# Performance work log

Measured on AMD Instinct MI355X. Metric: run time of the kernel, lower is better.

## Reference

```python
import jax, jax.numpy as jnp
import numpy as np

# ---- HashGridPlanesEncoder config (hybrid-k-planes) ----
NUM_LEVELS = 16
LEVEL_DIM = 2
BASE_RES = 16
DESIRED_RES = 2048
LOG2_HASHMAP = 19
D = 2  # grid_nd: each plane encoder is a 2D hash grid
N_PTS = 1048576
COO_COMBS = [(0, 1), (0, 2), (1, 2)]
HASH_PRIME_1 = 2654435761  # torch-ngp fast_hash prime for dim 1 (dim 0 prime is 1)


def _level_constants():
    # Mirrors torch-ngp GridEncoder offset/resolution computation.
    pls = 2.0 ** (np.log2(DESIRED_RES / BASE_RES) / (NUM_LEVELS - 1))
    max_params = 2 ** LOG2_HASHMAP
    scales, res, sizes, offs = [], [], [], [0]
    for l in range(NUM_LEVELS):
        s = BASE_RES * pls ** l - 1.0          # kernel: scale = exp2(l*S + H) - 1
        r = int(np.ceil(s)) + 1                # kernel: resolution = ceil(scale) + 1
        p = min(max_params, (r + 1) ** D)      # align_corners=False -> (res+1)^D
        p = int(np.ceil(p / 8) * 8)            # round up to multiple of 8
        scales.append(s); res.append(r); sizes.append(p); offs.append(offs[-1] + p)
    return (np.array(scales, np.float32), np.array(res, np.int64),
            np.array(sizes, np.int64), np.array(offs[:-1], np.int64), offs[-1])


SCALES, RES, SIZES, OFFSETS, TOTAL_PARAMS = _level_constants()
USE_HASH = ((RES + 1) ** D) > SIZES  # static per-level: dense linear index vs spatial hash


def _encode_plane(x2, table):
    """x2: [N,2] coords in [0,1]; table: [TOTAL_PARAMS, LEVEL_DIM]. Returns [N, L*C]."""
    n = x2.shape[0]
    scales = jnp.asarray(SCALES)
    pos = x2[:, None, :] * scales[None, :, None] + 0.5           # [N,L,2] (align_corners=False)
    pg_f = jnp.floor(pos)
    frac = pos - pg_f                                            # [N,L,2]
    pg = pg_f.astype(jnp.uint32)
    corners = jnp.array([[0, 0], [1, 0], [0, 1], [1, 1]], jnp.uint32)  # [4,2]
    cpos = pg[:, :, None, :] + corners[None, None]               # [N,L,4,2]
    cmask = corners.astype(bool)[None, None]                     # [1,1,4,2]
    w = jnp.where(cmask, frac[:, :, None, :], 1.0 - frac[:, :, None, :]).prod(-1)  # [N,L,4]
    stride1 = jnp.asarray((RES + 1).astype(np.uint32))           # [L]
    linear = cpos[..., 0] + cpos[..., 1] * stride1[None, :, None]
    hashed = cpos[..., 0] ^ (cpos[..., 1] * jnp.uint32(HASH_PRIME_1))  # uint32 wrap-around
    idx = jnp.where(jnp.asarray(USE_HASH)[None, :, None], hashed, linear)
    idx = idx % jnp.asarray(SIZES.astype(np.uint32))[None, :, None]
    idx = (idx + jnp.asarray(OFFSETS.astype(np.uint32))[None, :, None]).astype(jnp.int32)
    feats = table[idx]                                           # [N,L,4,C] gather
    out = (w[..., None] * feats).sum(axis=2)                     # [N,L,C] bilinear interp
    return out.reshape(n, NUM_LEVELS * LEVEL_DIM)


def setup_inputs() -> dict:
    key = jax.random.key(0)
    kp, k0, k1, k2 = jax.random.split(key, 4)
    pts = jax.random.uniform(kp, (N_PTS, 3), dtype=jnp.float32)  # coords (treated as in [-1,1] domain)
    std = 1e-4  # GridEncoder init: embeddings.uniform_(-1e-4, 1e-4)
    mk = lambda k: jax.random.uniform(k, (TOTAL_PARAMS, LEVEL_DIM), jnp.float32, -std, std)
    return {"pts": pts, "table_xy": mk(k0), "table_xz": mk(k1), "table_yz": mk(k2)}


def reference(pts, table_xy, table_xz, table_yz):
    # GridEncoder.forward normalizes inputs: (x + bound) / (2*bound), bound=1
    u = (pts + 1.0) * 0.5
    tables = (table_xy, table_xz, table_yz)
    out = _encode_plane(u[:, list(COO_COMBS[0])], tables[0])
    for comb, tab in zip(COO_COMBS[1:], tables[1:]):
        out = out + _encode_plane(u[:, list(comb)], tab)
    return out
```

## Files before the change

### kernel.cpp

```cpp
#include <hip/hip_runtime.h>
#include <hip/hip_fp16.h>
#include <cmath>

#define NLEV 16
#define HASH_START 12
#define HMASK ((1u << 19) - 1u)
#define HASH_PRIME 2654435761u
#define LDS_WORDS 14160

typedef float    f4 __attribute__((ext_vector_type(4)));
typedef unsigned u4 __attribute__((ext_vector_type(4)));

struct LvlC {
  float scale[NLEV];
  unsigned stride[NLEV];
  unsigned offset[NLEV];
};

__device__ __forceinline__ float2 h2f(unsigned u) {
  return __half22float2(__builtin_bit_cast(__half2, u));
}
__device__ __forceinline__ void nt_store4(float* p, float a, float b, float c, float d) {
  f4 v = {a, b, c, d};
  __builtin_nontemporal_store(v, reinterpret_cast<f4*>(p));
}

__global__ __launch_bounds__(256) void k_convert(
    const float2* __restrict__ t0, const float2* __restrict__ t1,
    const float2* __restrict__ t2, unsigned* __restrict__ dst, unsigned total)
{
  unsigned g = blockIdx.x * 256 + threadIdx.x;
  unsigned stp = gridDim.x * 256;
  unsigned tot3 = 3u * total;
  for (unsigned e = g; e < tot3; e += stp) {
    const float2* src; unsigned i = e;
    if (i < total)            { src = t0; }
    else if (i < 2u * total)  { src = t1; i -= total; }
    else                      { src = t2; i -= 2u * total; }
    float2 v = src[i];
    __half2 h = __floats2half2_rn(v.x, v.y);
    __builtin_nontemporal_store(__builtin_bit_cast(unsigned, h), dst + e);
  }
}

__global__ __launch_bounds__(256) void k_dense1011(
    const float* __restrict__ pts, const unsigned* __restrict__ tab,
    unsigned* __restrict__ s10, unsigned* __restrict__ s11,
    LvlC lc, unsigned total, int half)
{
  int t = blockIdx.x * 256 + threadIdx.x;
  if (t >= half) return;
  const int idx[2] = {t, t + half};

  float ua[2][3], ub[2][3];
#pragma unroll
  for (int k = 0; k < 2; ++k) {
    float u0 = (pts[3 * idx[k] + 0] + 1.f) * .5f;
    float u1 = (pts[3 * idx[k] + 1] + 1.f) * .5f;
    float u2 = (pts[3 * idx[k] + 2] + 1.f) * .5f;
    ua[k][0] = u0; ub[k][0] = u1;
    ua[k][1] = u0; ub[k][1] = u2;
    ua[k][2] = u1; ub[k][2] = u2;
  }

  uint2 g[2][2][3][2];
  float rx[2][2][3], ry[2][2][3];
#pragma unroll
  for (int k = 0; k < 2; ++k)
#pragma unroll
    for (int l = 0; l < 2; ++l) {
      const float sc = lc.scale[10 + l];
      const unsigned st = lc.stride[10 + l], o = lc.offset[10 + l];
#pragma unroll
      for (int p = 0; p < 3; ++p) {
        float px = ua[k][p] * sc + .5f, py = ub[k][p] * sc + .5f;
        float fx = floorf(px), fy = floorf(py);
        rx[k][l][p] = px - fx; ry[k][l][p] = py - fy;
        unsigned i00 = (unsigned)fx + (unsigned)fy * st + o;
        const unsigned* tp = tab + (size_t)p * total;
        g[k][l][p][0] = *reinterpret_cast<const uint2*>(tp + i00);
        g[k][l][p][1] = *reinterpret_cast<const uint2*>(tp + i00 + st);
      }
    }

#pragma unroll
  for (int k = 0; k < 2; ++k)
#pragma unroll
    for (int l = 0; l < 2; ++l) {
      float s0 = 0.f, s1 = 0.f;
#pragma unroll
      for (int p = 0; p < 3; ++p) {
        float x = rx[k][l][p], y = ry[k][l][p];
        float w00 = (1.f - x) * (1.f - y), w10 = x * (1.f - y);
        float w01 = (1.f - x) * y,          w11 = x * y;
        float2 f00 = h2f(g[k][l][p][0].x), f10 = h2f(g[k][l][p][0].y);
        float2 f01 = h2f(g[k][l][p][1].x), f11 = h2f(g[k][l][p][1].y);
        s0 += w00 * f00.x + w10 * f10.x + w01 * f01.x + w11 * f11.x;
        s1 += w00 * f00.y + w10 * f10.y + w01 * f01.y + w11 * f11.y;
      }
      unsigned hv = __builtin_bit_cast(unsigned, __floats2half2_rn(s0, s1));
      unsigned* sl = l ? s11 : s10;
      __builtin_nontemporal_store(hv, sl + idx[k]);
    }
}

__global__ __launch_bounds__(256) void k_hash_lvl(
    const float* __restrict__ pts, const unsigned* __restrict__ tab,
    unsigned* __restrict__ slice, float sc, unsigned o, unsigned total, int half)
{
  int t = blockIdx.x * 256 + threadIdx.x;
  if (t >= half) return;
  const int idx[2] = {t, t + half};

  float ua[2][3], ub[2][3];
#pragma unroll
  for (int k = 0; k < 2; ++k) {
    float u0 = (pts[3 * idx[k] + 0] + 1.f) * .5f;
    float u1 = (pts[3 * idx[k] + 1] + 1.f) * .5f;
    float u2 = (pts[3 * idx[k] + 2] + 1.f) * .5f;
    ua[k][0] = u0; ub[k][0] = u1;
    ua[k][1] = u0; ub[k][1] = u2;
    ua[k][2] = u1; ub[k][2] = u2;
  }

  unsigned g[2][3][4];
  float rx[2][3], ry[2][3];
#pragma unroll
  for (int k = 0; k < 2; ++k)
#pragma unroll
    for (int p = 0; p < 3; ++p) {
      float px = ua[k][p] * sc + .5f, py = ub[k][p] * sc + .5f;
      float fx = floorf(px), fy = floorf(py);
      rx[k][p] = px - fx; ry[k][p] = py - fy;
      unsigned x0 = (unsigned)fx, y0 = (unsigned)fy;
      unsigned hy0 = y0 * HASH_PRIME, hy1 = hy0 + HASH_PRIME;
      const unsigned* tp = tab + (size_t)p * total + o;
      g[k][p][0] = tp[(x0 ^ hy0) & HMASK];
      g[k][p][1] = tp[((x0 + 1u) ^ hy0) & HMASK];
      g[k][p][2] = tp[(x0 ^ hy1) & HMASK];
      g[k][p][3] = tp[((x0 + 1u) ^ hy1) & HMASK];
    }

#pragma unroll
  for (int k = 0; k < 2; ++k) {
    float s0 = 0.f, s1 = 0.f;
#pragma unroll
    for (int p = 0; p < 3; ++p) {
      float x = rx[k][p], y = ry[k][p];
      float w00 = (1.f - x) * (1.f - y), w10 = x * (1.f - y);
      float w01 = (1.f - x) * y,          w11 = x * y;
      float2 f00 = h2f(g[k][p][0]), f10 = h2f(g[k][p][1]);
      float2 f01 = h2f(g[k][p][2]), f11 = h2f(g[k][p][3]);
      s0 += w00 * f00.x + w10 * f10.x + w01 * f01.x + w11 * f11.x;
      s1 += w00 * f00.y + w10 * f10.y + w01 * f01.y + w11 * f11.y;
    }
    __builtin_nontemporal_store(
        __builtin_bit_cast(unsigned, __floats2half2_rn(s0, s1)), slice + idx[k]);
  }
}

__global__ __launch_bounds__(256) void k_final(
    const float* __restrict__ pts, const unsigned* __restrict__ tab,
    const unsigned* __restrict__ slices,
    float* __restrict__ out, LvlC lc, unsigned total, int n)
{
  __shared__ unsigned lds[LDS_WORDS];
  int i = blockIdx.x * 256 + threadIdx.x;

  float u0 = (pts[3 * i + 0] + 1.f) * .5f;
  float u1 = (pts[3 * i + 1] + 1.f) * .5f;
  float u2 = (pts[3 * i + 2] + 1.f) * .5f;
  const float ua[3] = {u0, u0, u1}, ub[3] = {u1, u2, u2};

  float res[12];
#pragma unroll
  for (int j = 0; j < 12; ++j) res[j] = 0.f;

  for (int p = 0; p < 3; ++p) {
    if (p) __syncthreads();
    const u4* src = reinterpret_cast<const u4*>(tab + (size_t)p * total);
    for (unsigned e = threadIdx.x; e < LDS_WORDS / 4; e += 256)
      reinterpret_cast<u4*>(lds)[e] = src[e];
    __syncthreads();
#pragma unroll
    for (int l = 0; l < 6; ++l) {
      float px = ua[p] * lc.scale[l] + .5f, py = ub[p] * lc.scale[l] + .5f;
      float fx = floorf(px), fy = floorf(py);
      float x = px - fx, y = py - fy;
      unsigned st = lc.stride[l];
      unsigned i00 = (unsigned)fx + (unsigned)fy * st + lc.offset[l];
      float2 f00 = h2f(lds[i00]),      f10 = h2f(lds[i00 + 1]);
      float2 f01 = h2f(lds[i00 + st]), f11 = h2f(lds[i00 + st + 1]);
      float w00 = (1.f - x) * (1.f - y), w10 = x * (1.f - y);
      float w01 = (1.f - x) * y,          w11 = x * y;
      res[2 * l + 0] += w00 * f00.x + w10 * f10.x + w01 * f01.x + w11 * f11.x;
      res[2 * l + 1] += w00 * f00.y + w10 * f10.y + w01 * f01.y + w11 * f11.y;
    }
  }

  uint2 g[4][3][2];
  float gx[4][3], gy[4][3];
#pragma unroll
  for (int l = 0; l < 4; ++l) {
    const float sc = lc.scale[6 + l];
    const unsigned st = lc.stride[6 + l], o = lc.offset[6 + l];
#pragma unroll
    for (int p = 0; p < 3; ++p) {
      float px = ua[p] * sc + .5f, py = ub[p] * sc + .5f;
      float fx = floorf(px), fy = floorf(py);
      gx[l][p] = px - fx; gy[l][p] = py - fy;
      unsigned i00 = (unsigned)fx + (unsigned)fy * st + o;
      const unsigned* tp = tab + (size_t)p * total;
      g[l][p][0] = *reinterpret_cast<const uint2*>(tp + i00);
      g[l][p][1] = *reinterpret_cast<const uint2*>(tp + i00 + st);
    }
  }
  unsigned sl[6];
#pragma unroll
  for (int j = 0; j < 6; ++j) sl[j] = slices[(size_t)j * n + i];

  float res69[8];
#pragma unroll
  for (int l = 0; l < 4; ++l) {
    float s0 = 0.f, s1 = 0.f;
#pragma unroll
    for (int p = 0; p < 3; ++p) {
      float x = gx[l][p], y = gy[l][p];
      float w00 = (1.f - x) * (1.f - y), w10 = x * (1.f - y);
      float w01 = (1.f - x) * y,          w11 = x * y;
      float2 f00 = h2f(g[l][p][0].x), f10 = h2f(g[l][p][0].y);
      float2 f01 = h2f(g[l][p][1].x), f11 = h2f(g[l][p][1].y);
      s0 += w00 * f00.x + w10 * f10.x + w01 * f01.x + w11 * f11.x;
      s1 += w00 * f00.y + w10 * f10.y + w01 * f01.y + w11 * f11.y;
    }
    res69[2 * l] = s0; res69[2 * l + 1] = s1;
  }

  float v[32];
#pragma unroll
  for (int j = 0; j < 12; ++j) v[j] = res[j];
#pragma unroll
  for (int j = 0; j < 8; ++j) v[12 + j] = res69[j];
#pragma unroll
  for (int j = 0; j < 6; ++j) {
    float2 f = h2f(sl[j]);
    v[20 + 2 * j] = f.x; v[20 + 2 * j + 1] = f.y;
  }
  float* orow = out + (size_t)i * 32;
#pragma unroll
  for (int j = 0; j < 8; ++j)
    nt_store4(orow + 4 * j, v[4 * j], v[4 * j + 1], v[4 * j + 2], v[4 * j + 3]);
}

__global__ __launch_bounds__(256) void k_fallback(
    const float* __restrict__ pts, const float2* __restrict__ txy,
    const float2* __restrict__ txz, const float2* __restrict__ tyz,
    float* __restrict__ out, LvlC lc, int n)
{
  int i = blockIdx.x * 256 + threadIdx.x;
  if (i >= n) return;
  float u0 = (pts[3 * i + 0] + 1.f) * .5f;
  float u1 = (pts[3 * i + 1] + 1.f) * .5f;
  float u2 = (pts[3 * i + 2] + 1.f) * .5f;
  const float ua[3] = {u0, u0, u1}, ub[3] = {u1, u2, u2};
  const float2* tabs[3] = {txy, txz, tyz};
  float acc[32];
#pragma unroll
  for (int j = 0; j < 32; ++j) acc[j] = 0.f;
#pragma unroll
  for (int l = 0; l < NLEV; ++l) {
    const float sc = lc.scale[l];
    const unsigned o = lc.offset[l], s = lc.stride[l];
#pragma unroll
    for (int p = 0; p < 3; ++p) {
      const float2* t = tabs[p];
      float px = ua[p] * sc + .5f, py = ub[p] * sc + .5f;
      float fx = floorf(px), fy = floorf(py);
      float rx = px - fx, ry = py - fy;
      unsigned x0 = (unsigned)fx, y0 = (unsigned)fy;
      float w00 = (1.f - rx) * (1.f - ry), w10 = rx * (1.f - ry);
      float w01 = (1.f - rx) * ry,          w11 = rx * ry;
      float2 f00, f10, f01, f11;
      if (l >= HASH_START) {
        unsigned hy0 = y0 * HASH_PRIME, hy1 = hy0 + HASH_PRIME;
        f00 = t[o + ((x0 ^ hy0) & HMASK)];
        f10 = t[o + (((x0 + 1u) ^ hy0) & HMASK)];
        f01 = t[o + ((x0 ^ hy1) & HMASK)];
        f11 = t[o + (((x0 + 1u) ^ hy1) & HMASK)];
      } else {
        unsigned i00 = x0 + y0 * s;
        float4 r0 = *reinterpret_cast<const float4*>(t + o + i00);
        float4 r1 = *reinterpret_cast<const float4*>(t + o + i00 + s);
        f00 = make_float2(r0.x, r0.y); f10 = make_float2(r0.z, r0.w);
        f01 = make_float2(r1.x, r1.y); f11 = make_float2(r1.z, r1.w);
      }
      acc[2 * l + 0] += w00 * f00.x + w10 * f10.x + w01 * f01.x + w11 * f11.x;
      acc[2 * l + 1] += w00 * f00.y + w10 * f10.y + w01 * f01.y + w11 * f11.y;
    }
  }
  float* orow = out + (size_t)i * 32;
#pragma unroll
  for (int j = 0; j < 8; ++j)
    nt_store4(orow + 4 * j, acc[4 * j], acc[4 * j + 1], acc[4 * j + 2], acc[4 * j + 3]);
}

static unsigned compute_levels(LvlC* lc)
{
  const double pls = std::pow(2.0, std::log2(2048.0 / 16.0) / 15.0);
  unsigned long long off = 0;
  for (int l = 0; l < NLEV; ++l) {
    double s = 16.0 * std::pow(pls, (double)l) - 1.0;
    lc->scale[l] = (float)s;
    long long r = (long long)std::ceil(s) + 1;
    long long dense = (r + 1) * (r + 1);
    long long sz = dense < (1LL << 19) ? dense : (1LL << 19);
    sz = ((sz + 7) / 8) * 8;
    lc->stride[l] = (unsigned)(r + 1);
    lc->offset[l] = (unsigned)off;
    off += (unsigned long long)sz;
  }
  return (unsigned)off;
}

extern "C" void kernel_launch(void* const* d_in, const int* in_sizes, int n_in,
                              void* d_out, int out_size, void* d_ws, size_t ws_size,
                              hipStream_t stream) {
  const float*  pts = (const float*)d_in[0];
  const float2* txy = (const float2*)d_in[1];
  const float2* txz = (const float2*)d_in[2];
  const float2* tyz = (const float2*)d_in[3];
  float* out = (float*)d_out;
  int n = in_sizes[0] / 3;

  LvlC lc;
  unsigned total = compute_levels(&lc);

  size_t tab_bytes = (size_t)3 * total * 4;
  size_t tab_al = (tab_bytes + 255) & ~(size_t)255;
  size_t need = tab_al + (size_t)6 * n * 4;

  bool ok = (n % 512 == 0) && (lc.offset[6] == LDS_WORDS) && (ws_size >= need);
  for (int l = HASH_START; l < NLEV; ++l) {
    unsigned sz = ((l + 1 < NLEV) ? lc.offset[l + 1] : total) - lc.offset[l];
    ok = ok && (sz == (1u << 19));
  }

  int block = 256;
  int grid = (n + block - 1) / block;
  if (!ok) {
    k_fallback<<<grid, block, 0, stream>>>(pts, txy, txz, tyz, out, lc, n);
    return;
  }

  unsigned* tab16 = (unsigned*)d_ws;
  unsigned* slices = (unsigned*)((char*)d_ws + tab_al);

  int half = n / 2;
  int gridh = half / block;

  k_convert<<<2048, 256, 0, stream>>>(txy, txz, tyz, tab16, total);
  k_dense1011<<<gridh, block, 0, stream>>>(pts, tab16, slices, slices + (size_t)n,
                                           lc, total, half);
  for (int l = HASH_START; l < NLEV; ++l)
    k_hash_lvl<<<gridh, block, 0, stream>>>(pts, tab16, slices + (size_t)(l - 10) * n,
                                            lc.scale[l], lc.offset[l], total, half);
  k_final<<<grid, block, 0, stream>>>(pts, tab16, slices, out, lc, total, n);
}
```

Baseline: 397.3 us.

## Fuse all per-level kernels into one monolithic kernel with paired hash loads

Replaces the dense-pair kernel, four per-level hash kernels and the final kernel with a single 512-thread kernel that computes all 16 levels per point and writes the output directly. This removes the intermediate fp16 slice buffers (write and reread of 6 slices) and several kernel launches. Hash lookups with even x0 now fetch both corners with one 8-byte load, since x0 and x0+1 then differ only in bit 0 of the hashed index. The trade-off is that per-level kernels, which kept each hash table hot in L2 one level at a time, are gone, so all four 2MB-per-plane hash levels compete for cache at once, and register pressure per thread rises.

```diff
diff --git a/kernel.cpp b/kernel.cpp
--- a/kernel.cpp
+++ b/kernel.cpp
@@ -43,143 +43,119 @@
   }
 }
 
-__global__ __launch_bounds__(256) void k_dense1011(
-    const float* __restrict__ pts, const unsigned* __restrict__ tab,
-    unsigned* __restrict__ s10, unsigned* __restrict__ s11,
-    LvlC lc, unsigned total, int half)
-{
-  int t = blockIdx.x * 256 + threadIdx.x;
-  if (t >= half) return;
-  const int idx[2] = {t, t + half};
-
-  float ua[2][3], ub[2][3];
-#pragma unroll
-  for (int k = 0; k < 2; ++k) {
-    float u0 = (pts[3 * idx[k] + 0] + 1.f) * .5f;
-    float u1 = (pts[3 * idx[k] + 1] + 1.f) * .5f;
-    float u2 = (pts[3 * idx[k] + 2] + 1.f) * .5f;
-    ua[k][0] = u0; ub[k][0] = u1;
-    ua[k][1] = u0; ub[k][1] = u2;
-    ua[k][2] = u1; ub[k][2] = u2;
-  }
-
-  uint2 g[2][2][3][2];
-  float rx[2][2][3], ry[2][2][3];
-#pragma unroll
-  for (int k = 0; k < 2; ++k)
-#pragma unroll
-    for (int l = 0; l < 2; ++l) {
-      const float sc = lc.scale[10 + l];
-      const unsigned st = lc.stride[10 + l], o = lc.offset[10 + l];
-#pragma unroll
-      for (int p = 0; p < 3; ++p) {
-        float px = ua[k][p] * sc + .5f, py = ub[k][p] * sc + .5f;
-        float fx = floorf(px), fy = floorf(py);
-        rx[k][l][p] = px - fx; ry[k][l][p] = py - fy;
-        unsigned i00 = (unsigned)fx + (unsigned)fy * st + o;
-        const unsigned* tp = tab + (size_t)p * total;
-        g[k][l][p][0] = *reinterpret_cast<const uint2*>(tp + i00);
-        g[k][l][p][1] = *reinterpret_cast<const uint2*>(tp + i00 + st);
-      }
-    }
-
-#pragma unroll
-  for (int k = 0; k < 2; ++k)
-#pragma unroll
-    for (int l = 0; l < 2; ++l) {
-      float s0 = 0.f, s1 = 0.f;
-#pragma unroll
-      for (int p = 0; p < 3; ++p) {
-        float x = rx[k][l][p], y = ry[k][l][p];
-        float w00 = (1.f - x) * (1.f - y), w10 = x * (1.f - y);
-        float w01 = (1.f - x) * y,          w11 = x * y;
-        float2 f00 = h2f(g[k][l][p][0].x), f10 = h2f(g[k][l][p][0].y);
-        float2 f01 = h2f(g[k][l][p][1].x), f11 = h2f(g[k][l][p][1].y);
-        s0 += w00 * f00.x + w10 * f10.x + w01 * f01.x + w11 * f11.x;
-        s1 += w00 * f00.y + w10 * f10.y + w01 * f01.y + w11 * f11.y;
-      }
-      unsigned hv = __builtin_bit_cast(unsigned, __floats2half2_rn(s0, s1));
-      unsigned* sl = l ? s11 : s10;
-      __builtin_nontemporal_store(hv, sl + idx[k]);
-    }
-}
-
-__global__ __launch_bounds__(256) void k_hash_lvl(
-    const float* __restrict__ pts, const unsigned* __restrict__ tab,
-    unsigned* __restrict__ slice, float sc, unsigned o, unsigned total, int half)
-{
-  int t = blockIdx.x * 256 + threadIdx.x;
-  if (t >= half) return;
-  const int idx[2] = {t, t + half};
-
-  float ua[2][3], ub[2][3];
-#pragma unroll
-  for (int k = 0; k < 2; ++k) {
-    float u0 = (pts[3 * idx[k] + 0] + 1.f) * .5f;
-    float u1 = (pts[3 * idx[k] + 1] + 1.f) * .5f;
-    float u2 = (pts[3 * idx[k] + 2] + 1.f) * .5f;
-    ua[k][0] = u0; ub[k][0] = u1;
-    ua[k][1] = u0; ub[k][1] = u2;
-    ua[k][2] = u1; ub[k][2] = u2;
-  }
-
+__device__ __forceinline__ void dense_pair(
+    const unsigned* __restrict__ tab, size_t total, const LvlC& lc, int l0,
+    const float* ua, const float* ub, float* res4)
+{
+  uint2 g[2][3][2];
+  float rx[2][3], ry[2][3];
+#pragma unroll
+  for (int h = 0; h < 2; ++h) {
+    const float sc = lc.scale[l0 + h];
+    const unsigned st = lc.stride[l0 + h], o = lc.offset[l0 + h];
+#pragma unroll
+    for (int p = 0; p < 3; ++p) {
+      float px = ua[p] * sc + .5f, py = ub[p] * sc + .5f;
+      float fx = floorf(px), fy = floorf(py);
+      rx[h][p] = px - fx; ry[h][p] = py - fy;
+      unsigned i00 = (unsigned)fx + (unsigned)fy * st + o;
+      const unsigned* tp = tab + (size_t)p * total;
+      g[h][p][0] = *reinterpret_cast<const uint2*>(tp + i00);
+      g[h][p][1] = *reinterpret_cast<const uint2*>(tp + i00 + st);
+    }
+  }
+#pragma unroll
+  for (int h = 0; h < 2; ++h) {
+    float s0 = 0.f, s1 = 0.f;
+#pragma unroll
+    for (int p = 0; p < 3; ++p) {
+      float x = rx[h][p], y = ry[h][p];
+      float w00 = (1.f - x) * (1.f - y), w10 = x * (1.f - y);
+      float w01 = (1.f - x) * y,          w11 = x * y;
+      float2 f00 = h2f(g[h][p][0].x), f10 = h2f(g[h][p][0].y);
+      float2 f01 = h2f(g[h][p][1].x), f11 = h2f(g[h][p][1].y);
+      s0 += w00 * f00.x + w10 * f10.x + w01 * f01.x + w11 * f11.x;
+      s1 += w00 * f00.y + w10 * f10.y + w01 * f01.y + w11 * f11.y;
+    }
+    res4[2 * h + 0] = s0; res4[2 * h + 1] = s1;
+  }
+}
+
+__device__ __forceinline__ void hash_row(
+    const unsigned* __restrict__ tp, unsigned x0, unsigned hy,
+    unsigned& g0, unsigned& g1)
+{
+  unsigned a0 = (x0 ^ hy) & HMASK;
+  if ((x0 & 1u) == 0u) {
+    uint2 v = *reinterpret_cast<const uint2*>(tp + (a0 & ~1u));
+    bool hi = (a0 & 1u) != 0u;
+    g0 = hi ? v.y : v.x;
+    g1 = hi ? v.x : v.y;
+  } else {
+    g0 = tp[a0];
+    g1 = tp[((x0 + 1u) ^ hy) & HMASK];
+  }
+}
+
+__device__ __forceinline__ void hash_pair(
+    const unsigned* __restrict__ tab, size_t total, const LvlC& lc, int l0,
+    const float* ua, const float* ub, float* res4)
+{
   unsigned g[2][3][4];
   float rx[2][3], ry[2][3];
 #pragma unroll
-  for (int k = 0; k < 2; ++k)
-#pragma unroll
-    for (int p = 0; p < 3; ++p) {
-      float px = ua[k][p] * sc + .5f, py = ub[k][p] * sc + .5f;
-      float fx = floorf(px), fy = floorf(py);
-      rx[k][p] = px - fx; ry[k][p] = py - fy;
+  for (int h = 0; h < 2; ++h) {
+    const float sc = lc.scale[l0 + h];
+    const unsigned o = lc.offset[l0 + h];
+#pragma unroll
+    for (int p = 0; p < 3; ++p) {
+      float px = ua[p] * sc + .5f, py = ub[p] * sc + .5f;
+      float fx = floorf(px), fy = floorf(py);
+      rx[h][p] = px - fx; ry[h][p] = py - fy;
       unsigned x0 = (unsigned)fx, y0 = (unsigned)fy;
       unsigned hy0 = y0 * HASH_PRIME, hy1 = hy0 + HASH_PRIME;
       const unsigned* tp = tab + (size_t)p * total + o;
-      g[k][p][0] = tp[(x0 ^ hy0) & HMASK];
-      g[k][p][1] = tp[((x0 + 1u) ^ hy0) & HMASK];
-      g[k][p][2] = tp[(x0 ^ hy1) & HMASK];
-      g[k][p][3] = tp[((x0 + 1u) ^ hy1) & HMASK];
-    }
-
-#pragma unroll
-  for (int k = 0; k < 2; ++k) {
+      hash_row(tp, x0, hy0, g[h][p][0], g[h][p][1]);
+      hash_row(tp, x0, hy1, g[h][p][2], g[h][p][3]);
+    }
+  }
+#pragma unroll
+  for (int h = 0; h < 2; ++h) {
     float s0 = 0.f, s1 = 0.f;
 #pragma unroll
     for (int p = 0; p < 3; ++p) {
-      float x = rx[k][p], y = ry[k][p];
+      float x = rx[h][p], y = ry[h][p];
       float w00 = (1.f - x) * (1.f - y), w10 = x * (1.f - y);
       float w01 = (1.f - x) * y,          w11 = x * y;
-      float2 f00 = h2f(g[k][p][0]), f10 = h2f(g[k][p][1]);
-      float2 f01 = h2f(g[k][p][2]), f11 = h2f(g[k][p][3]);
+      float2 f00 = h2f(g[h][p][0]), f10 = h2f(g[h][p][1]);
+      float2 f01 = h2f(g[h][p][2]), f11 = h2f(g[h][p][3]);
       s0 += w00 * f00.x + w10 * f10.x + w01 * f01.x + w11 * f11.x;
       s1 += w00 * f00.y + w10 * f10.y + w01 * f01.y + w11 * f11.y;
     }
-    __builtin_nontemporal_store(
-        __builtin_bit_cast(unsigned, __floats2half2_rn(s0, s1)), slice + idx[k]);
-  }
-}
-
-__global__ __launch_bounds__(256) void k_final(
+    res4[2 * h + 0] = s0; res4[2 * h + 1] = s1;
+  }
+}
+
+__global__ __launch_bounds__(512) void k_mono(
     const float* __restrict__ pts, const unsigned* __restrict__ tab,
-    const unsigned* __restrict__ slices,
     float* __restrict__ out, LvlC lc, unsigned total, int n)
 {
   __shared__ unsigned lds[LDS_WORDS];
-  int i = blockIdx.x * 256 + threadIdx.x;
+  int i = blockIdx.x * 512 + threadIdx.x;
 
   float u0 = (pts[3 * i + 0] + 1.f) * .5f;
   float u1 = (pts[3 * i + 1] + 1.f) * .5f;
   float u2 = (pts[3 * i + 2] + 1.f) * .5f;
   const float ua[3] = {u0, u0, u1}, ub[3] = {u1, u2, u2};
 
-  float res[12];
+  float res[32];
 #pragma unroll
   for (int j = 0; j < 12; ++j) res[j] = 0.f;
 
   for (int p = 0; p < 3; ++p) {
     if (p) __syncthreads();
     const u4* src = reinterpret_cast<const u4*>(tab + (size_t)p * total);
-    for (unsigned e = threadIdx.x; e < LDS_WORDS / 4; e += 256)
+    for (unsigned e = threadIdx.x; e < LDS_WORDS / 4; e += 512)
       reinterpret_cast<u4*>(lds)[e] = src[e];
     __syncthreads();
 #pragma unroll
@@ -198,58 +174,16 @@
     }
   }
 
-  uint2 g[4][3][2];
-  float gx[4][3], gy[4][3];
-#pragma unroll
-  for (int l = 0; l < 4; ++l) {
-    const float sc = lc.scale[6 + l];
-    const unsigned st = lc.stride[6 + l], o = lc.offset[6 + l];
-#pragma unroll
-    for (int p = 0; p < 3; ++p) {
-      float px = ua[p] * sc + .5f, py = ub[p] * sc + .5f;
-      float fx = floorf(px), fy = floorf(py);
-      gx[l][p] = px - fx; gy[l][p] = py - fy;
-      unsigned i00 = (unsigned)fx + (unsigned)fy * st + o;
-      const unsigned* tp = tab + (size_t)p * total;
-      g[l][p][0] = *reinterpret_cast<const uint2*>(tp + i00);
-      g[l][p][1] = *reinterpret_cast<const uint2*>(tp + i00 + st);
-    }
-  }
-  unsigned sl[6];
-#pragma unroll
-  for (int j = 0; j < 6; ++j) sl[j] = slices[(size_t)j * n + i];
-
-  float res69[8];
-#pragma unroll
-  for (int l = 0; l < 4; ++l) {
-    float s0 = 0.f, s1 = 0.f;
-#pragma unroll
-    for (int p = 0; p < 3; ++p) {
-      float x = gx[l][p], y = gy[l][p];
-      float w00 = (1.f - x) * (1.f - y), w10 = x * (1.f - y);
-      float w01 = (1.f - x) * y,          w11 = x * y;
-      float2 f00 = h2f(g[l][p][0].x), f10 = h2f(g[l][p][0].y);
-      float2 f01 = h2f(g[l][p][1].x), f11 = h2f(g[l][p][1].y);
-      s0 += w00 * f00.x + w10 * f10.x + w01 * f01.x + w11 * f11.x;
-      s1 += w00 * f00.y + w10 * f10.y + w01 * f01.y + w11 * f11.y;
-    }
-    res69[2 * l] = s0; res69[2 * l + 1] = s1;
-  }
-
-  float v[32];
-#pragma unroll
-  for (int j = 0; j < 12; ++j) v[j] = res[j];
-#pragma unroll
-  for (int j = 0; j < 8; ++j) v[12 + j] = res69[j];
-#pragma unroll
-  for (int j = 0; j < 6; ++j) {
-    float2 f = h2f(sl[j]);
-    v[20 + 2 * j] = f.x; v[20 + 2 * j + 1] = f.y;
-  }
+  dense_pair(tab, total, lc, 6,  ua, ub, res + 12);
+  dense_pair(tab, total, lc, 8,  ua, ub, res + 16);
+  dense_pair(tab, total, lc, 10, ua, ub, res + 20);
+  hash_pair (tab, total, lc, 12, ua, ub, res + 24);
+  hash_pair (tab, total, lc, 14, ua, ub, res + 28);
+
   float* orow = out + (size_t)i * 32;
 #pragma unroll
   for (int j = 0; j < 8; ++j)
-    nt_store4(orow + 4 * j, v[4 * j], v[4 * j + 1], v[4 * j + 2], v[4 * j + 3]);
+    nt_store4(orow + 4 * j, res[4 * j], res[4 * j + 1], res[4 * j + 2], res[4 * j + 3]);
 }
 
 __global__ __launch_bounds__(256) void k_fallback(
@@ -335,34 +269,20 @@
   LvlC lc;
   unsigned total = compute_levels(&lc);
 
-  size_t tab_bytes = (size_t)3 * total * 4;
-  size_t tab_al = (tab_bytes + 255) & ~(size_t)255;
-  size_t need = tab_al + (size_t)6 * n * 4;
-
+  size_t need = (size_t)3 * total * 4;
   bool ok = (n % 512 == 0) && (lc.offset[6] == LDS_WORDS) && (ws_size >= need);
   for (int l = HASH_START; l < NLEV; ++l) {
     unsigned sz = ((l + 1 < NLEV) ? lc.offset[l + 1] : total) - lc.offset[l];
     ok = ok && (sz == (1u << 19));
   }
 
-  int block = 256;
-  int grid = (n + block - 1) / block;
   if (!ok) {
-    k_fallback<<<grid, block, 0, stream>>>(pts, txy, txz, tyz, out, lc, n);
+    int grid = (n + 255) / 256;
+    k_fallback<<<grid, 256, 0, stream>>>(pts, txy, txz, tyz, out, lc, n);
     return;
   }
 
   unsigned* tab16 = (unsigned*)d_ws;
-  unsigned* slices = (unsigned*)((char*)d_ws + tab_al);
-
-  int half = n / 2;
-  int gridh = half / block;
-
   k_convert<<<2048, 256, 0, stream>>>(txy, txz, tyz, tab16, total);
-  k_dense1011<<<gridh, block, 0, stream>>>(pts, tab16, slices, slices + (size_t)n,
-                                           lc, total, half);
-  for (int l = HASH_START; l < NLEV; ++l)
-    k_hash_lvl<<<gridh, block, 0, stream>>>(pts, tab16, slices + (size_t)(l - 10) * n,
-                                            lc.scale[l], lc.offset[l], total, half);
-  k_final<<<grid, block, 0, stream>>>(pts, tab16, slices, out, lc, total, n);
-}
+  k_mono<<<n / 512, 512, 0, stream>>>(pts, tab16, out, lc, total, n);
+}
```

After: 682.9 us. 1.72x slower.
